# Kernel optimization log

Measured on AMD Instinct MI355X. Metric: run time of the kernel, lower is better.

Reference implementation:

```python
import jax, jax.numpy as jnp
import numpy as np

N_HEAD = 16
HEAD_SIZE = 64
N_EMBD = 1024
B, T = 4, 2048
THETA = 10000.0


def _rope_cos_sin(t_len, dim):
    # freqs: (dim//2,), angles: (T, dim//2)
    inv = 1.0 / (THETA ** (jnp.arange(0, dim, 2, dtype=jnp.float32) / dim))
    ang = jnp.arange(t_len, dtype=jnp.float32)[:, None] * inv[None, :]
    return jnp.cos(ang), jnp.sin(ang)


def _apply_rope(x, cos, sin):
    # x: (B, H, T, hs) -> complex-pair rotation over last dim
    xr = x.reshape(*x.shape[:-1], -1, 2)
    x0, x1 = xr[..., 0], xr[..., 1]
    c = cos[None, None, :, :]
    s = sin[None, None, :, :]
    o0 = x0 * c - x1 * s
    o1 = x0 * s + x1 * c
    return jnp.stack([o0, o1], axis=-1).reshape(x.shape)


def setup_inputs() -> dict:
    key = jax.random.key(0)
    ks = jax.random.split(key, 5)
    scale = 1.0 / np.sqrt(N_EMBD)
    return {
        "x": jax.random.normal(ks[0], (B, T, N_EMBD), dtype=jnp.float32),
        "Wq": jax.random.normal(ks[1], (N_EMBD, N_HEAD * HEAD_SIZE), dtype=jnp.float32) * scale,
        "Wk": jax.random.normal(ks[2], (N_EMBD, N_HEAD * HEAD_SIZE), dtype=jnp.float32) * scale,
        "Wv": jax.random.normal(ks[3], (N_EMBD, N_HEAD * HEAD_SIZE), dtype=jnp.float32) * scale,
        "Wp": jax.random.normal(ks[4], (N_HEAD * HEAD_SIZE, N_EMBD), dtype=jnp.float32) * scale,
        "bp": jnp.zeros((N_EMBD,), dtype=jnp.float32),
    }


def reference(x, Wq, Wk, Wv, Wp, bp):
    Bx, Tx, C = x.shape
    q = (x @ Wq).reshape(Bx, Tx, N_HEAD, HEAD_SIZE).transpose(0, 2, 1, 3)
    k = (x @ Wk).reshape(Bx, Tx, N_HEAD, HEAD_SIZE).transpose(0, 2, 1, 3)
    v = (x @ Wv).reshape(Bx, Tx, N_HEAD, HEAD_SIZE).transpose(0, 2, 1, 3)
    cos, sin = _rope_cos_sin(Tx, HEAD_SIZE)
    q = _apply_rope(q, cos, sin)
    k = _apply_rope(k, cos, sin)
    wei = jnp.einsum('bhqd,bhkd->bhqk', q, k) * (HEAD_SIZE ** -0.5)
    causal = jnp.tril(jnp.ones((Tx, Tx), dtype=bool))
    wei = jnp.where(causal[None, None, :, :], wei, -jnp.inf)
    wei = jax.nn.softmax(wei, axis=-1)
    out = jnp.einsum('bhqk,bhkd->bhqd', wei, v)
    out = out.transpose(0, 2, 1, 3).reshape(Bx, Tx, N_HEAD * HEAD_SIZE)
    return out @ Wp + bp
```

## Files before the change

### kernel.cpp

```cpp
#include <hip/hip_runtime.h>
#include <hip/hip_bf16.h>

#define NH 16
#define HS 64
#define CE 1024
#define BB 4
#define TT 2048

typedef __bf16 bf16;
typedef __bf16 v8bf __attribute__((ext_vector_type(8)));
typedef __bf16 v4bf __attribute__((ext_vector_type(4)));
typedef __bf16 v2bf __attribute__((ext_vector_type(2)));
typedef float v4f __attribute__((ext_vector_type(4)));
typedef float v16f __attribute__((ext_vector_type(16)));

#define GLD16(gp, lp)                                                              \
    __builtin_amdgcn_global_load_lds((const __attribute__((address_space(1))) void*)(gp), \
                                     (__attribute__((address_space(3))) void*)(lp), 16, 0, 0)

#define FENCE() __builtin_amdgcn_sched_barrier(0)
#define BARRIER() { FENCE(); __builtin_amdgcn_s_barrier(); FENCE(); }
#define VM4()  { asm volatile("s_waitcnt vmcnt(4)" ::: "memory"); FENCE(); }
#define VM8()  { asm volatile("s_waitcnt vmcnt(8)" ::: "memory"); FENCE(); }
#define VM0()  { asm volatile("s_waitcnt vmcnt(0)" ::: "memory"); FENCE(); }

__global__ __launch_bounds__(256) void prep_kernel(const float* __restrict__ x,
                                                   const float* __restrict__ W0,
                                                   const float* __restrict__ W1,
                                                   const float* __restrict__ W2,
                                                   const float* __restrict__ W3,
                                                   bf16* __restrict__ xb,
                                                   float2* __restrict__ csQ,
                                                   float2* __restrict__ csK,
                                                   bf16* __restrict__ dqkv,
                                                   bf16* __restrict__ dp) {
    __shared__ bf16 tile[64][66];
    const int bid = blockIdx.x;
    const int tid = threadIdx.x;
    if (bid < 4096) {
        int idx = (bid * 256 + tid) * 8;
        const float4* xp = (const float4*)(x + idx);
        float4 a = xp[0], b = xp[1];
        v8bf o;
        o[0] = (bf16)a.x; o[1] = (bf16)a.y; o[2] = (bf16)a.z; o[3] = (bf16)a.w;
        o[4] = (bf16)b.x; o[5] = (bf16)b.y; o[6] = (bf16)b.z; o[7] = (bf16)b.w;
        *(v8bf*)(xb + idx) = o;
    } else if (bid < 4352) {
        int idx = (bid - 4096) * 256 + tid;
        int t = idx >> 5, i = idx & 31;
        float inv = exp2f(-0.41524101186092034f * (float)i);
        float ang = (float)t * inv;
        float s, c;
        sincosf(ang, &s, &c);
        const float QS = 0.18033688011112042f;
        csK[idx] = make_float2(c, s);
        csQ[idx] = make_float2(c * QS, s * QS);
    } else {
        int idx = bid - 4352;
        int z = idx >> 8, rem = idx & 255;
        const float* W = (z == 0) ? W0 : (z == 1) ? W1 : (z == 2) ? W2 : W3;
        bf16* Wt = (z < 3) ? (dqkv + (size_t)z * 1024 * CE) : dp;
        int k0 = (rem & 15) * 64;
        int n0 = (rem >> 4) * 64;
        int tx = tid & 63;
        int ty = tid >> 6;
        for (int s = 0; s < 16; s++) {
            int r = s * 4 + ty;
            tile[r][tx] = (bf16)W[(size_t)(k0 + r) * CE + n0 + tx];
        }
        __syncthreads();
        for (int s = 0; s < 16; s++) {
            int r = s * 4 + ty;
            Wt[(size_t)(n0 + r) * CE + k0 + tx] = tile[tx][r];
        }
    }
}

#define GSTAGE(AD, BD, kk) {                                                        \
    _Pragma("unroll") for (int p = 0; p < 4; p++)                                   \
        GLD16(Ag + (kk) + (size_t)(p * 32) * CE, (AD) + p * 2048);                  \
    _Pragma("unroll") for (int p = 0; p < 4; p++)                                   \
        GLD16(Bg + (kk) + (size_t)(p * 32) * CE, (BD) + p * 2048); }

#define GCOMPUTE(ASrc, BSrc)                                                        \
    _Pragma("unroll")                                                               \
    for (int kh = 0; kh < 2; kh++) {                                                \
        v8bf af[4], bfr[4];                                                         \
        for (int i = 0; i < 4; i++) {                                               \
            int row = wr * 64 + i * 16 + lane15;                                    \
            af[i] = *(const v8bf*)(&ASrc[row * 64 + (((kh * 4 + quad) ^ (lane15 & 7)) * 8)]); \
        }                                                                           \
        for (int j = 0; j < 4; j++) {                                               \
            int row = wc * 64 + j * 16 + lane15;                                    \
            bfr[j] = *(const v8bf*)(&BSrc[row * 64 + (((kh * 4 + quad) ^ (lane15 & 7)) * 8)]); \
        }                                                                           \
        for (int i = 0; i < 4; i++)                                                 \
            for (int j = 0; j < 4; j++)                                             \
                acc[i][j] = __builtin_amdgcn_mfma_f32_16x16x32_bf16(af[i], bfr[j], acc[i][j], 0, 0, 0); \
    }

template <int MODE>
__global__ __launch_bounds__(256) void gemm_bt(const bf16* __restrict__ A,
                                               const bf16* __restrict__ Bt,
                                               bf16* __restrict__ Qb_, bf16* __restrict__ Kb_,
                                               bf16* __restrict__ Vt_,
                                               float* __restrict__ Pout,
                                               const float* __restrict__ bias,
                                               const float2* __restrict__ csQ,
                                               const float2* __restrict__ csK) {
    __shared__ __align__(16) bf16 As0[128 * 64];
    __shared__ __align__(16) bf16 Bs0[128 * 64];
    __shared__ __align__(16) bf16 As1[128 * 64];
    __shared__ __align__(16) bf16 Bs1[128 * 64];
    const int tid = threadIdx.x;
    const int lane = tid & 63, wave = tid >> 6;
    const int lane15 = lane & 15, quad = lane >> 4;
    const int wr = wave >> 1, wc = wave & 1;
    const int m0 = blockIdx.y * 128;
    const int n0 = blockIdx.x * 128;

    v4f acc[4][4] = {};

    const int cm = tid >> 3;
    const int ck = ((tid & 7) ^ (cm & 7)) * 8;
    const bf16* Ag = A + (size_t)(m0 + cm) * CE + ck;
    const bf16* Bg = Bt + (size_t)(n0 + cm) * CE + ck;
    bf16* aD0 = &As0[wave * 512];
    bf16* bD0 = &Bs0[wave * 512];
    bf16* aD1 = &As1[wave * 512];
    bf16* bD1 = &Bs1[wave * 512];

    GSTAGE(aD0, bD0, 0);
    for (int k0 = 0; k0 < CE; k0 += 128) {
        GSTAGE(aD1, bD1, k0 + 64);
        VM8(); BARRIER();
        GCOMPUTE(As0, Bs0);
        BARRIER();
        GSTAGE(aD0, bD0, (k0 + 128) & 1023);
        VM8(); BARRIER();
        GCOMPUTE(As1, Bs1);
        BARRIER();
    }
    VM0();

    for (int i = 0; i < 4; i++) {
        for (int j = 0; j < 4; j++) {
            int gmb = m0 + wr * 64 + i * 16 + quad * 4;
            int gn = n0 + wc * 64 + j * 16 + lane15;
            if (MODE == 1) {
                float bb = bias[gn];
                for (int r = 0; r < 4; r++)
                    Pout[(size_t)(gmb + r) * CE + gn] = acc[i][j][r] + bb;
            } else {
                int w = gn >> 10;
                int n = gn & 1023;
                int hh = n >> 6, d = n & 63;
                if (w < 2) {
                    bf16* out = w ? Kb_ : Qb_;
                    const float2* csRow = (w ? csK : csQ) + (d >> 1);
                    const int par = gn & 1;
                    const int dbase = d & ~1;
                    const int b = gmb >> 11, tbase = gmb & 2047;
                    const float xv0 = acc[i][j][0], xv1 = acc[i][j][1];
                    const float xv2 = acc[i][j][2], xv3 = acc[i][j][3];
                    const float pv0 = __shfl_xor(xv0, 1), pv1 = __shfl_xor(xv1, 1);
                    const float pv2 = __shfl_xor(xv2, 1), pv3 = __shfl_xor(xv3, 1);
                    const float xa = par ? xv2 : xv0, pa = par ? pv2 : pv0;
                    const float xb2 = par ? xv3 : xv1, pb = par ? pv3 : pv1;
                    const float ua = par ? pa : xa, va = par ? xa : pa;
                    const float ub = par ? pb : xb2, vb = par ? xb2 : pb;
                    const int ta = tbase + (par << 1), tb = ta + 1;
                    const float2 csa = csRow[ta * 32];
                    const float2 csb = csRow[tb * 32];
                    v2bf sa, sb;
                    sa[0] = (bf16)(ua * csa.x - va * csa.y);
                    sa[1] = (bf16)(ua * csa.y + va * csa.x);
                    sb[0] = (bf16)(ub * csb.x - vb * csb.y);
                    sb[1] = (bf16)(ub * csb.y + vb * csb.x);
                    bf16* rowp = out + ((size_t)(b * NH + hh)) * TT * HS + dbase;
                    *(v2bf*)(rowp + (size_t)ta * HS) = sa;
                    *(v2bf*)(rowp + (size_t)tb * HS) = sb;
                } else {
                    int b = gmb >> 11, t = gmb & 2047;
                    v4bf pack;
                    for (int r = 0; r < 4; r++) pack[r] = (bf16)acc[i][j][r];
                    *(v4bf*)(&Vt_[(((size_t)(b * NH + hh)) * HS + d) * TT + t]) = pack;
                }
            }
        }
    }
}

#define ASTAGE(KD, VD, kv) {                                        \
    GLD16(kg + (size_t)(kv) * HS, (KD));                            \
    GLD16(kg + (size_t)((kv) + 32) * HS, (KD) + 2048);              \
    GLD16(vg + (kv), (VD));                                         \
    GLD16(vg + (kv) + 32 * TT, (VD) + 2048); }

#define ACOMPUTE(KS, VS, KVB)                                                       \
    _Pragma("unroll")                                                               \
    for (int sub = 0; sub < 2; sub++) {                                             \
        const int kvs = (KVB) + sub * 32;                                           \
        if (kvs > q0) break;                                                        \
        const bool diag = (kvs == q0);                                              \
        v16f s = {};                                                                \
        __builtin_amdgcn_s_setprio(1);                                              \
        for (int m = 0; m < 4; m++) {                                               \
            v8bf afr = *(const v8bf*)(&KS[(sub * 32 + lane31) * 64 +                \
                                          (((m << 1) | h) ^ (lane31 & 7)) * 8]);    \
            s = __builtin_amdgcn_mfma_f32_32x32x16_bf16(afr, qf[m], s, 0, 0, 0);    \
        }                                                                           \
        __builtin_amdgcn_s_setprio(0);                                              \
        float p[16];                                                                \
        if (diag) {                                                                 \
            for (int r = 0; r < 16; r++) {                                          \
                int kvr = (r & 3) + 8 * (r >> 2) + 4 * h;                           \
                p[r] = exp2f((kvr <= lane31) ? s[r] : -3.0e38f);                    \
            }                                                                       \
        } else {                                                                    \
            for (int r = 0; r < 16; r++) p[r] = exp2f(s[r]);                        \
        }                                                                           \
        float a8[8];                                                                \
        for (int r = 0; r < 8; r++) a8[r] = p[r] + p[r + 8];                        \
        l_i += ((a8[0] + a8[1]) + (a8[2] + a8[3])) + ((a8[4] + a8[5]) + (a8[6] + a8[7])); \
        union { v4bf v; unsigned long long u; } ch[4];                              \
        for (int g = 0; g < 4; g++)                                                 \
            for (int rr = 0; rr < 4; rr++)                                          \
                ch[g].v[rr] = (bf16)p[g * 4 + rr];                                  \
        __builtin_amdgcn_s_setprio(1);                                              \
        for (int t2 = 0; t2 < 2; t2++) {                                            \
            unsigned long long mine0 = ch[2 * t2].u, mine1 = ch[2 * t2 + 1].u;      \
            unsigned long long send = h ? mine0 : mine1;                            \
            unsigned long long recv = __shfl_xor(send, 32);                         \
            union { v8bf v; unsigned long long u[2]; } bfr2;                        \
            bfr2.u[0] = h ? recv : mine0;                                           \
            bfr2.u[1] = h ? mine1 : recv;                                           \
            int cidx = (((sub << 2) + (t2 << 1) + h) ^ (lane31 & 7)) * 8;           \
            v8bf va0 = *(const v8bf*)(&VS[lane31 * 64 + cidx]);                     \
            o0 = __builtin_amdgcn_mfma_f32_32x32x16_bf16(va0, bfr2.v, o0, 0, 0, 0); \
            v8bf va1 = *(const v8bf*)(&VS[(32 + lane31) * 64 + cidx]);              \
            o1 = __builtin_amdgcn_mfma_f32_32x32x16_bf16(va1, bfr2.v, o1, 0, 0, 0); \
        }                                                                           \
        __builtin_amdgcn_s_setprio(0);                                              \
    }

__global__ __launch_bounds__(256, 4) void attn_kernel(const bf16* __restrict__ Qb,
                                                      const bf16* __restrict__ Kb,
                                                      const bf16* __restrict__ Vt,
                                                      bf16* __restrict__ Ob) {
    __shared__ __align__(16) bf16 Ks0[64 * 64];
    __shared__ __align__(16) bf16 Vs0[64 * 64];
    __shared__ __align__(16) bf16 Ks1[64 * 64];
    __shared__ __align__(16) bf16 Vs1[64 * 64];
    const int tid = threadIdx.x, lane = tid & 63, wave = tid >> 6;
    const int lane31 = lane & 31, h = lane >> 5;
    const int bh = blockIdx.x & 63;
    const int qb = 15 - (int)(blockIdx.x >> 6);
    const int q0 = qb * 128 + wave * 32;
    const bf16* Qp = Qb + (size_t)bh * TT * HS;
    const bf16* Kp = Kb + (size_t)bh * TT * HS;
    const bf16* Vp = Vt + (size_t)bh * HS * TT;

    v8bf qf[4];
    for (int m = 0; m < 4; m++)
        qf[m] = *(const v8bf*)(Qp + (size_t)(q0 + lane31) * HS + m * 16 + h * 8);

    v16f o0 = {}, o1 = {};
    float l_i = 0.f;

    const int kr = tid >> 3, kc = tid & 7;
    const bf16* kg = Kp + kr * HS + ((kc ^ (kr & 7)) * 8);
    const bf16* vg = Vp + (size_t)kr * TT + ((kc ^ (kr & 7)) * 8);
    bf16* ksD0 = &Ks0[wave * 512];
    bf16* vsD0 = &Vs0[wave * 512];
    bf16* ksD1 = &Ks1[wave * 512];
    bf16* vsD1 = &Vs1[wave * 512];

    const int kv_max = qb * 128 + 96;
    ASTAGE(ksD0, vsD0, 0);
    for (int kv0 = 0; kv0 <= kv_max; kv0 += 128) {
        ASTAGE(ksD1, vsD1, kv0 + 64);
        VM4(); BARRIER();
        ACOMPUTE(Ks0, Vs0, kv0);
        BARRIER();
        ASTAGE(ksD0, vsD0, (kv0 + 128) & 2047);
        VM4(); BARRIER();
        ACOMPUTE(Ks1, Vs1, kv0 + 64);
        BARRIER();
    }
    VM0();

    const int b = bh >> 4, hh = bh & 15;
    const int q = q0 + lane31;
    float lt = l_i + __shfl_xor(l_i, 32);
    float invl = 1.f / lt;
    bf16* outRow = Ob + ((size_t)(b * TT + q)) * CE + hh * HS;
    for (int g = 0; g < 4; g++) {
        v4bf w0, w1;
        for (int rr = 0; rr < 4; rr++) {
            w0[rr] = (bf16)(o0[g * 4 + rr] * invl);
            w1[rr] = (bf16)(o1[g * 4 + rr] * invl);
        }
        *(v4bf*)(outRow + g * 8 + h * 4) = w0;
        *(v4bf*)(outRow + 32 + g * 8 + h * 4) = w1;
    }
}

extern "C" void kernel_launch(void* const* d_in, const int* in_sizes, int n_in,
                              void* d_out, int out_size, void* d_ws, size_t ws_size,
                              hipStream_t stream) {
    const float* x  = (const float*)d_in[0];
    const float* Wq = (const float*)d_in[1];
    const float* Wk = (const float*)d_in[2];
    const float* Wv = (const float*)d_in[3];
    const float* Wp = (const float*)d_in[4];
    const float* bp = (const float*)d_in[5];
    char* ws = (char*)d_ws;
    const size_t MB = 1024 * 1024;
    bf16* Xb    = (bf16*)(ws);
    bf16* WqkvT = (bf16*)(ws + 16 * MB);
    bf16* WpT   = (bf16*)(ws + 22 * MB);
    bf16* Qb    = (bf16*)(ws + 24 * MB);
    bf16* Kb    = (bf16*)(ws + 40 * MB);
    bf16* Vt    = (bf16*)(ws + 56 * MB);
    bf16* Ob    = (bf16*)(ws + 72 * MB);
    float2* csQ = (float2*)(ws + 72 * MB);
    float2* csK = (float2*)(ws + 72 * MB + 512 * 1024);

    prep_kernel<<<dim3(5376), dim3(256), 0, stream>>>(x, Wq, Wk, Wv, Wp, Xb, csQ, csK,
                                                      WqkvT, WpT);

    gemm_bt<0><<<dim3(24, 64), dim3(256), 0, stream>>>(Xb, WqkvT, Qb, Kb, Vt, nullptr, nullptr,
                                                       csQ, csK);

    attn_kernel<<<dim3(1024), dim3(256), 0, stream>>>(Qb, Kb, Vt, Ob);

    gemm_bt<1><<<dim3(8, 64), dim3(256), 0, stream>>>(Ob, WpT, nullptr, nullptr, nullptr,
                                                      (float*)d_out, bp, nullptr, nullptr);
}
```

Baseline: 256.2 us.

## Process two 32-row query tiles per wave to reuse K/V fragments

Each wave now handles 64 query rows as two 32-row halves, so the K and V fragments read from shared memory are loaded into registers once and used by both halves. Blocks cover 256 query rows and the grid is halved to 512 blocks, with launch bounds lowered to 2 blocks per SM to leave room for the doubled accumulators. This is meant to cut LDS reads per MFMA and the number of K/V staging passes, at the cost of higher register pressure, lower occupancy, and coarser causal load balance across blocks.

```diff
diff --git a/kernel.cpp b/kernel.cpp
--- a/kernel.cpp
+++ b/kernel.cpp
@@ -197,54 +197,65 @@
     GLD16(vg + (kv), (VD));                                         \
     GLD16(vg + (kv) + 32 * TT, (VD) + 2048); }
 
-#define ACOMPUTE(KS, VS, KVB)                                                       \
-    _Pragma("unroll")                                                               \
-    for (int sub = 0; sub < 2; sub++) {                                             \
-        const int kvs = (KVB) + sub * 32;                                           \
-        if (kvs > q0) break;                                                        \
-        const bool diag = (kvs == q0);                                              \
+#define AHALF(QF, O0, O1, LI, QBASE) {                                              \
+    if (kvs <= (QBASE)) {                                                           \
+        const bool diag = (kvs == (QBASE));                                         \
         v16f s = {};                                                                \
         __builtin_amdgcn_s_setprio(1);                                              \
-        for (int m = 0; m < 4; m++) {                                               \
-            v8bf afr = *(const v8bf*)(&KS[(sub * 32 + lane31) * 64 +                \
-                                          (((m << 1) | h) ^ (lane31 & 7)) * 8]);    \
-            s = __builtin_amdgcn_mfma_f32_32x32x16_bf16(afr, qf[m], s, 0, 0, 0);    \
-        }                                                                           \
+        _Pragma("unroll") for (int m = 0; m < 4; m++)                               \
+            s = __builtin_amdgcn_mfma_f32_32x32x16_bf16(kf[m], QF[m], s, 0, 0, 0);  \
         __builtin_amdgcn_s_setprio(0);                                              \
         float p[16];                                                                \
         if (diag) {                                                                 \
-            for (int r = 0; r < 16; r++) {                                          \
+            _Pragma("unroll") for (int r = 0; r < 16; r++) {                        \
                 int kvr = (r & 3) + 8 * (r >> 2) + 4 * h;                           \
                 p[r] = exp2f((kvr <= lane31) ? s[r] : -3.0e38f);                    \
             }                                                                       \
         } else {                                                                    \
-            for (int r = 0; r < 16; r++) p[r] = exp2f(s[r]);                        \
+            _Pragma("unroll") for (int r = 0; r < 16; r++) p[r] = exp2f(s[r]);      \
         }                                                                           \
         float a8[8];                                                                \
-        for (int r = 0; r < 8; r++) a8[r] = p[r] + p[r + 8];                        \
-        l_i += ((a8[0] + a8[1]) + (a8[2] + a8[3])) + ((a8[4] + a8[5]) + (a8[6] + a8[7])); \
+        _Pragma("unroll") for (int r = 0; r < 8; r++) a8[r] = p[r] + p[r + 8];      \
+        LI += ((a8[0] + a8[1]) + (a8[2] + a8[3])) + ((a8[4] + a8[5]) + (a8[6] + a8[7])); \
         union { v4bf v; unsigned long long u; } ch[4];                              \
-        for (int g = 0; g < 4; g++)                                                 \
+        _Pragma("unroll") for (int g = 0; g < 4; g++)                               \
             for (int rr = 0; rr < 4; rr++)                                          \
                 ch[g].v[rr] = (bf16)p[g * 4 + rr];                                  \
         __builtin_amdgcn_s_setprio(1);                                              \
-        for (int t2 = 0; t2 < 2; t2++) {                                            \
+        _Pragma("unroll") for (int t2 = 0; t2 < 2; t2++) {                          \
             unsigned long long mine0 = ch[2 * t2].u, mine1 = ch[2 * t2 + 1].u;      \
             unsigned long long send = h ? mine0 : mine1;                            \
             unsigned long long recv = __shfl_xor(send, 32);                         \
             union { v8bf v; unsigned long long u[2]; } bfr2;                        \
             bfr2.u[0] = h ? recv : mine0;                                           \
             bfr2.u[1] = h ? mine1 : recv;                                           \
+            O0 = __builtin_amdgcn_mfma_f32_32x32x16_bf16(va0[t2], bfr2.v, O0, 0, 0, 0); \
+            O1 = __builtin_amdgcn_mfma_f32_32x32x16_bf16(va1[t2], bfr2.v, O1, 0, 0, 0); \
+        }                                                                           \
+        __builtin_amdgcn_s_setprio(0);                                              \
+    }                                                                               \
+}
+
+#define ACOMPUTE(KS, VS, KVB)                                                       \
+    _Pragma("unroll")                                                               \
+    for (int sub = 0; sub < 2; sub++) {                                             \
+        const int kvs = (KVB) + sub * 32;                                           \
+        if (kvs > q0 + 32) break;                                                   \
+        v8bf kf[4];                                                                 \
+        _Pragma("unroll") for (int m = 0; m < 4; m++)                               \
+            kf[m] = *(const v8bf*)(&KS[(sub * 32 + lane31) * 64 +                   \
+                                       (((m << 1) | h) ^ (lane31 & 7)) * 8]);       \
+        v8bf va0[2], va1[2];                                                        \
+        _Pragma("unroll") for (int t2 = 0; t2 < 2; t2++) {                          \
             int cidx = (((sub << 2) + (t2 << 1) + h) ^ (lane31 & 7)) * 8;           \
-            v8bf va0 = *(const v8bf*)(&VS[lane31 * 64 + cidx]);                     \
-            o0 = __builtin_amdgcn_mfma_f32_32x32x16_bf16(va0, bfr2.v, o0, 0, 0, 0); \
-            v8bf va1 = *(const v8bf*)(&VS[(32 + lane31) * 64 + cidx]);              \
-            o1 = __builtin_amdgcn_mfma_f32_32x32x16_bf16(va1, bfr2.v, o1, 0, 0, 0); \
-        }                                                                           \
-        __builtin_amdgcn_s_setprio(0);                                              \
-    }
-
-__global__ __launch_bounds__(256, 4) void attn_kernel(const bf16* __restrict__ Qb,
+            va0[t2] = *(const v8bf*)(&VS[lane31 * 64 + cidx]);                      \
+            va1[t2] = *(const v8bf*)(&VS[(32 + lane31) * 64 + cidx]);               \
+        }                                                                           \
+        AHALF(qfH, o0H, o1H, l_H, q0 + 32);                                         \
+        AHALF(qfL, o0L, o1L, l_L, q0);                                              \
+    }
+
+__global__ __launch_bounds__(256, 2) void attn_kernel(const bf16* __restrict__ Qb,
                                                       const bf16* __restrict__ Kb,
                                                       const bf16* __restrict__ Vt,
                                                       bf16* __restrict__ Ob) {
@@ -255,18 +266,20 @@
     const int tid = threadIdx.x, lane = tid & 63, wave = tid >> 6;
     const int lane31 = lane & 31, h = lane >> 5;
     const int bh = blockIdx.x & 63;
-    const int qb = 15 - (int)(blockIdx.x >> 6);
-    const int q0 = qb * 128 + wave * 32;
+    const int qb = 7 - (int)(blockIdx.x >> 6);
+    const int q0 = qb * 256 + wave * 64;
     const bf16* Qp = Qb + (size_t)bh * TT * HS;
     const bf16* Kp = Kb + (size_t)bh * TT * HS;
     const bf16* Vp = Vt + (size_t)bh * HS * TT;
 
-    v8bf qf[4];
-    for (int m = 0; m < 4; m++)
-        qf[m] = *(const v8bf*)(Qp + (size_t)(q0 + lane31) * HS + m * 16 + h * 8);
-
-    v16f o0 = {}, o1 = {};
-    float l_i = 0.f;
+    v8bf qfL[4], qfH[4];
+    for (int m = 0; m < 4; m++) {
+        qfL[m] = *(const v8bf*)(Qp + (size_t)(q0 + lane31) * HS + m * 16 + h * 8);
+        qfH[m] = *(const v8bf*)(Qp + (size_t)(q0 + 32 + lane31) * HS + m * 16 + h * 8);
+    }
+
+    v16f o0L = {}, o1L = {}, o0H = {}, o1H = {};
+    float l_L = 0.f, l_H = 0.f;
 
     const int kr = tid >> 3, kc = tid & 7;
     const bf16* kg = Kp + kr * HS + ((kc ^ (kr & 7)) * 8);
@@ -276,9 +289,9 @@
     bf16* ksD1 = &Ks1[wave * 512];
     bf16* vsD1 = &Vs1[wave * 512];
 
-    const int kv_max = qb * 128 + 96;
+    const int kv_end = (qb + 1) * 256;
     ASTAGE(ksD0, vsD0, 0);
-    for (int kv0 = 0; kv0 <= kv_max; kv0 += 128) {
+    for (int kv0 = 0; kv0 < kv_end; kv0 += 128) {
         ASTAGE(ksD1, vsD1, kv0 + 64);
         VM4(); BARRIER();
         ACOMPUTE(Ks0, Vs0, kv0);
@@ -291,18 +304,35 @@
     VM0();
 
     const int b = bh >> 4, hh = bh & 15;
-    const int q = q0 + lane31;
-    float lt = l_i + __shfl_xor(l_i, 32);
-    float invl = 1.f / lt;
-    bf16* outRow = Ob + ((size_t)(b * TT + q)) * CE + hh * HS;
-    for (int g = 0; g < 4; g++) {
-        v4bf w0, w1;
-        for (int rr = 0; rr < 4; rr++) {
-            w0[rr] = (bf16)(o0[g * 4 + rr] * invl);
-            w1[rr] = (bf16)(o1[g * 4 + rr] * invl);
-        }
-        *(v4bf*)(outRow + g * 8 + h * 4) = w0;
-        *(v4bf*)(outRow + 32 + g * 8 + h * 4) = w1;
+    {
+        const int q = q0 + lane31;
+        float lt = l_L + __shfl_xor(l_L, 32);
+        float invl = 1.f / lt;
+        bf16* outRow = Ob + ((size_t)(b * TT + q)) * CE + hh * HS;
+        for (int g = 0; g < 4; g++) {
+            v4bf w0, w1;
+            for (int rr = 0; rr < 4; rr++) {
+                w0[rr] = (bf16)(o0L[g * 4 + rr] * invl);
+                w1[rr] = (bf16)(o1L[g * 4 + rr] * invl);
+            }
+            *(v4bf*)(outRow + g * 8 + h * 4) = w0;
+            *(v4bf*)(outRow + 32 + g * 8 + h * 4) = w1;
+        }
+    }
+    {
+        const int q = q0 + 32 + lane31;
+        float lt = l_H + __shfl_xor(l_H, 32);
+        float invl = 1.f / lt;
+        bf16* outRow = Ob + ((size_t)(b * TT + q)) * CE + hh * HS;
+        for (int g = 0; g < 4; g++) {
+            v4bf w0, w1;
+            for (int rr = 0; rr < 4; rr++) {
+                w0[rr] = (bf16)(o0H[g * 4 + rr] * invl);
+                w1[rr] = (bf16)(o1H[g * 4 + rr] * invl);
+            }
+            *(v4bf*)(outRow + g * 8 + h * 4) = w0;
+            *(v4bf*)(outRow + 32 + g * 8 + h * 4) = w1;
+        }
     }
 }
 
@@ -333,7 +363,7 @@
     gemm_bt<0><<<dim3(24, 64), dim3(256), 0, stream>>>(Xb, WqkvT, Qb, Kb, Vt, nullptr, nullptr,
                                                        csQ, csK);
 
-    attn_kernel<<<dim3(1024), dim3(256), 0, stream>>>(Qb, Kb, Vt, Ob);
+    attn_kernel<<<dim3(512), dim3(256), 0, stream>>>(Qb, Kb, Vt, Ob);
 
     gemm_bt<1><<<dim3(8, 64), dim3(256), 0, stream>>>(Ob, WpT, nullptr, nullptr, nullptr,
                                                       (float*)d_out, bp, nullptr, nullptr);
```

Result: slower. 276.8 us (+8.0%).
